# Performance work log

Measured on AMD Instinct MI355X. Metric: run time of the kernel, lower is better.

The kernel has to match this reference:

```python
import jax, jax.numpy as jnp
import numpy as np

B, S, D, H, L = 32, 512, 512, 8, 6
NQ, FF, V, C = 8, 2048, 32000, 10
DK = D // H
EPS = 1e-5


def _layernorm(x, g, b):
    mu = jnp.mean(x, axis=-1, keepdims=True)
    var = jnp.mean(jnp.square(x - mu), axis=-1, keepdims=True)
    return (x - mu) * jax.lax.rsqrt(var + EPS) * g + b


def _pos_encoding(seq_len, dim):
    pos = jnp.arange(seq_len, dtype=jnp.float32)[:, None]
    div = jnp.exp(jnp.arange(0, dim, 2, dtype=jnp.float32) * (-jnp.log(10000.0) / dim))
    pe = jnp.zeros((seq_len, dim), dtype=jnp.float32)
    pe = pe.at[:, 0::2].set(jnp.sin(pos * div))
    pe = pe.at[:, 1::2].set(jnp.cos(pos * div))
    return pe


def setup_inputs() -> dict:
    key = jax.random.key(0)
    ks = jax.random.split(key, 16)
    sd = 0.02
    return {
        "x": jax.random.randint(ks[0], (B, S), 0, V),
        "emb": jax.random.normal(ks[1], (V, D), jnp.float32) * sd,
        "ln1_g": jnp.ones((L, D), jnp.float32),
        "ln1_b": jnp.zeros((L, D), jnp.float32),
        "ln2_g": jnp.ones((L, D), jnp.float32),
        "ln2_b": jnp.zeros((L, D), jnp.float32),
        "attn_w": jax.random.normal(ks[2], (L, D, D), jnp.float32) * sd,
        "attn_b": jnp.zeros((L, D), jnp.float32),
        "theta": jax.random.normal(ks[3], (L, NQ), jnp.float32),
        "ffn_w1": jax.random.normal(ks[4], (L, NQ, FF), jnp.float32) * sd,
        "ffn_b1": jnp.zeros((L, FF), jnp.float32),
        "ffn_w2": jax.random.normal(ks[5], (L, FF, D), jnp.float32) * sd,
        "ffn_b2": jnp.zeros((L, D), jnp.float32),
        "clf_w": jax.random.normal(ks[6], (D, C), jnp.float32) * sd,
        "clf_b": jnp.zeros((C,), jnp.float32),
    }


def reference(x, emb, ln1_g, ln1_b, ln2_g, ln2_b, attn_w, attn_b, theta,
              ffn_w1, ffn_b1, ffn_w2, ffn_b2, clf_w, clf_b):
    h = emb[x] + _pos_encoding(S, D)[None]  # [B,S,D]
    scale = 1.0 / jnp.sqrt(jnp.float32(DK))
    for l in range(L):
        # --- MultiHeadAttentionQuantum: q=k=v=reshape(x), no projections ---
        q = h.reshape(B, S, H, DK)
        scores = jnp.einsum('bihd,bjhd->bhij', q, q) * scale
        p = jax.nn.softmax(scores, axis=-1)
        attn = jnp.einsum('bhij,bjhd->bihd', p, q).reshape(B, S, D)
        attn = attn @ attn_w[l] + attn_b[l]
        h = _layernorm(h + attn, ln1_g[l], ln1_b[l])
        # --- FeedForwardQuantum: per-wire RX-encode -> RY(theta) -> <Z> = cos(x)cos(theta) ---
        qout = jnp.cos(h[..., :NQ]) * jnp.cos(theta[l])  # [B,S,NQ]
        f = jax.nn.relu(qout @ ffn_w1[l] + ffn_b1[l]) @ ffn_w2[l] + ffn_b2[l]
        h = _layernorm(h + f, ln2_g[l], ln2_b[l])
    pooled = jnp.mean(h, axis=1)  # [B,D]
    return pooled @ clf_w + clf_b  # [B,C]
```

## Files before the change

kernel.cpp:

```cpp
#include <hip/hip_runtime.h>
#include <hip/hip_bf16.h>
#include <math.h>

#define BB 32
#define SS 512
#define DD 512
#define HH 8
#define DK 64
#define LL 6
#define NQ 8
#define FF 2048
#define CC 10

typedef unsigned int uint;
typedef unsigned short ushort_t;
using bf16x8 = __attribute__((ext_vector_type(8))) short;
using f32x4  = __attribute__((ext_vector_type(4))) float;

#define MFMA(a, b, c) __builtin_amdgcn_mfma_f32_16x16x32_bf16((a), (b), (c), 0, 0, 0)

union U8 { ushort_t u[8]; bf16x8 v; };

__device__ inline ushort_t f2bf(float x) {
    uint u = __float_as_uint(x);
    u += 0x7FFFu + ((u >> 16) & 1u);
    return (ushort_t)(u >> 16);
}
__device__ inline void tsplit(float v, ushort_t& hi, ushort_t& lo) {
    uint u = __float_as_uint(v);
    hi = (ushort_t)(u >> 16);
    lo = f2bf(v - __uint_as_float(u & 0xFFFF0000u));
}
__device__ inline void tsplit_fast(float v, ushort_t& hi, ushort_t& lo) {
    uint u = __float_as_uint(v);
    hi = (ushort_t)(u >> 16);
    float res = v - __uint_as_float(u & 0xFFFF0000u);
    lo = (ushort_t)(__float_as_uint(res) >> 16);
}
__device__ inline uint packsplit(float v) {
    uint u = __float_as_uint(v) & 0xFFFF0000u;
    uint ru = __float_as_uint(v - __uint_as_float(u));
    ru += 0x7FFFu + ((ru >> 16) & 1u);
    return u | (ru >> 16);
}
__device__ inline float unpackf(uint u) {
    return __uint_as_float(u & 0xFFFF0000u) + __uint_as_float(u << 16);
}

__global__ __launch_bounds__(256) void embed_pe(const int* __restrict__ x,
                                                const float* __restrict__ emb,
                                                uint* __restrict__ Hp) {
    int idx = blockIdx.x * 256 + threadIdx.x;
    if (idx >= BB * SS * DD) return;
    int d = idx & (DD - 1);
    int s = (idx >> 9) & (SS - 1);
    int tok = x[idx >> 9];
    int i2 = d >> 1;
    float freq = expf((float)(2 * i2) * (-9.210340371976184f / (float)DD));
    float ang = (float)s * freq;
    float pe = (d & 1) ? cosf(ang) : sinf(ang);
    Hp[idx] = packsplit(emb[(size_t)tok * DD + d] + pe);
}

__global__ __launch_bounds__(256) void transpose_split_w(const float* __restrict__ in,
                                                         ushort_t* __restrict__ outh,
                                                         ushort_t* __restrict__ outl,
                                                         int K, int N) {
    __shared__ ushort_t th[64][68], tl[64][68];
    int nb = N >> 6;
    int k0 = ((int)blockIdx.x / nb) << 6;
    int n0 = ((int)blockIdx.x % nb) << 6;
    int t = threadIdx.x;
    int r = t >> 2, cb = (t & 3) << 4;
#pragma unroll
    for (int c = 0; c < 4; c++) {
        float4 v = *reinterpret_cast<const float4*>(&in[(size_t)(k0 + r) * N + n0 + cb + 4 * c]);
        float vv[4] = {v.x, v.y, v.z, v.w};
#pragma unroll
        for (int e = 0; e < 4; e++) {
            ushort_t hb, lb; tsplit(vv[e], hb, lb);
            th[r][cb + 4 * c + e] = hb;
            tl[r][cb + 4 * c + e] = lb;
        }
    }
    __syncthreads();
    int n = t >> 2, kb = (t & 3) << 4;
#pragma unroll
    for (int c = 0; c < 4; c++) {
        ushort4 oh, ol;
        oh.x = th[kb + 4 * c + 0][n]; ol.x = tl[kb + 4 * c + 0][n];
        oh.y = th[kb + 4 * c + 1][n]; ol.y = tl[kb + 4 * c + 1][n];
        oh.z = th[kb + 4 * c + 2][n]; ol.z = tl[kb + 4 * c + 2][n];
        oh.w = th[kb + 4 * c + 3][n]; ol.w = tl[kb + 4 * c + 3][n];
        *reinterpret_cast<ushort4*>(&outh[(size_t)(n0 + n) * K + k0 + kb + 4 * c]) = oh;
        *reinterpret_cast<ushort4*>(&outl[(size_t)(n0 + n) * K + k0 + kb + 4 * c]) = ol;
    }
}

__global__ __launch_bounds__(256) void prep_w1t(const float* __restrict__ W1all,
                                                ushort_t* __restrict__ outh,
                                                ushort_t* __restrict__ outl) {
    int l = blockIdx.y;
    int f = blockIdx.x * 256 + threadIdx.x;
    const float* W1 = W1all + (size_t)l * NQ * FF;
    U8 ph, pl;
#pragma unroll
    for (int n = 0; n < 8; n++) {
        ushort_t hb, lb; tsplit(W1[n * FF + f], hb, lb);
        ph.u[n] = hb; pl.u[n] = lb;
    }
    *reinterpret_cast<bf16x8*>(&outh[((size_t)l * FF + f) * 8]) = ph.v;
    *reinterpret_cast<bf16x8*>(&outl[((size_t)l * FF + f) * 8]) = pl.v;
}

__global__ __launch_bounds__(512, 4) void flash_attn_split(const uint* __restrict__ Hp,
                                                           ushort_t* __restrict__ outh,
                                                           ushort_t* __restrict__ outl) {
    __shared__ __align__(16) ushort_t Kh[64][72], Kl[64][72];
    __shared__ __align__(16) ushort_t Vh[64][72], Vl[64][72];
    __shared__ __align__(16) ushort_t Ph[128][72], Pl[128][72];

    int i0 = blockIdx.x * 128;
    int h0 = blockIdx.y * DK;
    int b  = blockIdx.z;
    const uint* baseH = Hp + (size_t)b * (SS * DD);

    int t = threadIdx.x;
    int w = t >> 6;
    int ln = t & 63;
    int l15 = ln & 15, lh = ln >> 4;

    bf16x8 aqh0, aqh1, aql0, aql1;
    {
        int row = i0 + w * 16 + l15;
        const uint* src = &baseH[(size_t)row * DD + h0 + lh * 8];
        uint4 p0 = *reinterpret_cast<const uint4*>(src);
        uint4 p1 = *reinterpret_cast<const uint4*>(src + 4);
        uint4 p2 = *reinterpret_cast<const uint4*>(src + 32);
        uint4 p3 = *reinterpret_cast<const uint4*>(src + 36);
        uint a0[8] = {p0.x, p0.y, p0.z, p0.w, p1.x, p1.y, p1.z, p1.w};
        uint a1[8] = {p2.x, p2.y, p2.z, p2.w, p3.x, p3.y, p3.z, p3.w};
        U8 h0u, l0u, h1u, l1u;
#pragma unroll
        for (int e = 0; e < 8; e++) {
            h0u.u[e] = (ushort_t)(a0[e] >> 16);
            l0u.u[e] = (ushort_t)(a0[e] & 0xFFFFu);
            h1u.u[e] = (ushort_t)(a1[e] >> 16);
            l1u.u[e] = (ushort_t)(a1[e] & 0xFFFFu);
        }
        aqh0 = h0u.v; aql0 = l0u.v; aqh1 = h1u.v; aql1 = l1u.v;
    }

    float m_[4], l_[4], al[4];
    f32x4 acc[4];
    f32x4 z4 = {0.f, 0.f, 0.f, 0.f};
#pragma unroll
    for (int r = 0; r < 4; r++) { m_[r] = -1e30f; l_[r] = 0.f; acc[r] = z4; }

    int kr = t >> 3, kcb = (t & 7) * 8;
    int vc = t & 7, vr = t >> 3;

    for (int j0 = 0; j0 < SS; j0 += 64) {
        __syncthreads();
        {
            const uint* src = &baseH[(size_t)(j0 + kr) * DD + h0 + kcb];
            uint4 p0 = *reinterpret_cast<const uint4*>(src);
            uint4 p1 = *reinterpret_cast<const uint4*>(src + 4);
            uint a[8] = {p0.x, p0.y, p0.z, p0.w, p1.x, p1.y, p1.z, p1.w};
            U8 kh, kl;
#pragma unroll
            for (int e = 0; e < 8; e++) {
                kh.u[e] = (ushort_t)(a[e] >> 16);
                kl.u[e] = (ushort_t)(a[e] & 0xFFFFu);
            }
            *reinterpret_cast<bf16x8*>(&Kh[kr][kcb]) = kh.v;
            *reinterpret_cast<bf16x8*>(&Kl[kr][kcb]) = kl.v;
        }
        __syncthreads();
#pragma unroll
        for (int e = 0; e < 8; e++) {
            int d = vc + 8 * e;
            Vh[d][vr] = Kh[vr][d];
            Vl[d][vr] = Kl[vr][d];
        }
        f32x4 sc[4];
#pragma unroll
        for (int tt = 0; tt < 4; tt++) {
            bf16x8 bh0 = *reinterpret_cast<const bf16x8*>(&Kh[tt * 16 + l15][lh * 8]);
            bf16x8 bh1 = *reinterpret_cast<const bf16x8*>(&Kh[tt * 16 + l15][32 + lh * 8]);
            bf16x8 bl0 = *reinterpret_cast<const bf16x8*>(&Kl[tt * 16 + l15][lh * 8]);
            bf16x8 bl1 = *reinterpret_cast<const bf16x8*>(&Kl[tt * 16 + l15][32 + lh * 8]);
            f32x4 s = z4;
            s = MFMA(aqh0, bh0, s);
            s = MFMA(aqh1, bh1, s);
            s = MFMA(aqh0, bl0, s);
            s = MFMA(aqh1, bl1, s);
            s = MFMA(aql0, bh0, s);
            s = MFMA(aql1, bh1, s);
            sc[tt] = s * 0.125f;
        }
#pragma unroll
        for (int r = 0; r < 4; r++) {
            float mx = fmaxf(fmaxf(sc[0][r], sc[1][r]), fmaxf(sc[2][r], sc[3][r]));
            mx = fmaxf(mx, __shfl_xor(mx, 1));
            mx = fmaxf(mx, __shfl_xor(mx, 2));
            mx = fmaxf(mx, __shfl_xor(mx, 4));
            mx = fmaxf(mx, __shfl_xor(mx, 8));
            float nm = fmaxf(m_[r], mx);
            al[r] = __expf(m_[r] - nm);
            m_[r] = nm;
            float rs = 0.f;
#pragma unroll
            for (int tt = 0; tt < 4; tt++) {
                float p = __expf(sc[tt][r] - nm);
                sc[tt][r] = p;
                rs += p;
            }
            rs += __shfl_xor(rs, 1);
            rs += __shfl_xor(rs, 2);
            rs += __shfl_xor(rs, 4);
            rs += __shfl_xor(rs, 8);
            l_[r] = l_[r] * al[r] + rs;
        }
#pragma unroll
        for (int tt = 0; tt < 4; tt++)
#pragma unroll
            for (int r = 0; r < 4; r++) {
                ushort_t hb, lb; tsplit(sc[tt][r], hb, lb);
                Ph[w * 16 + lh * 4 + r][tt * 16 + l15] = hb;
                Pl[w * 16 + lh * 4 + r][tt * 16 + l15] = lb;
            }
        __syncthreads();
#pragma unroll
        for (int td = 0; td < 4; td++) {
            acc[td][0] *= al[0];
            acc[td][1] *= al[1];
            acc[td][2] *= al[2];
            acc[td][3] *= al[3];
        }
        bf16x8 aph0 = *reinterpret_cast<const bf16x8*>(&Ph[w * 16 + l15][lh * 8]);
        bf16x8 aph1 = *reinterpret_cast<const bf16x8*>(&Ph[w * 16 + l15][32 + lh * 8]);
        bf16x8 apl0 = *reinterpret_cast<const bf16x8*>(&Pl[w * 16 + l15][lh * 8]);
        bf16x8 apl1 = *reinterpret_cast<const bf16x8*>(&Pl[w * 16 + l15][32 + lh * 8]);
#pragma unroll
        for (int td = 0; td < 4; td++) {
            bf16x8 bvh0 = *reinterpret_cast<const bf16x8*>(&Vh[td * 16 + l15][lh * 8]);
            bf16x8 bvh1 = *reinterpret_cast<const bf16x8*>(&Vh[td * 16 + l15][32 + lh * 8]);
            bf16x8 bvl0 = *reinterpret_cast<const bf16x8*>(&Vl[td * 16 + l15][lh * 8]);
            bf16x8 bvl1 = *reinterpret_cast<const bf16x8*>(&Vl[td * 16 + l15][32 + lh * 8]);
            acc[td] = MFMA(aph0, bvh0, acc[td]);
            acc[td] = MFMA(aph1, bvh1, acc[td]);
            acc[td] = MFMA(aph0, bvl0, acc[td]);
            acc[td] = MFMA(aph1, bvl1, acc[td]);
            acc[td] = MFMA(apl0, bvh0, acc[td]);
            acc[td] = MFMA(apl1, bvh1, acc[td]);
        }
    }

#pragma unroll
    for (int r = 0; r < 4; r++) {
        float inv = 1.f / l_[r];
        int row = i0 + w * 16 + lh * 4 + r;
#pragma unroll
        for (int td = 0; td < 4; td++) {
            float o = acc[td][r] * inv;
            ushort_t hb, lb; tsplit(o, hb, lb);
            size_t idx = (size_t)b * SS * DD + (size_t)row * DD + h0 + td * 16 + l15;
            outh[idx] = hb;
            outl[idx] = lb;
        }
    }
}

__global__ __launch_bounds__(512, 4) void gemm_split(const ushort_t* __restrict__ Ah,
                                                     const ushort_t* __restrict__ Al,
                                                     const ushort_t* __restrict__ Bth,
                                                     const ushort_t* __restrict__ Btl,
                                                     const float* __restrict__ bias,
                                                     float* __restrict__ C,
                                                     int M, int N, int K) {
    __shared__ __align__(16) ushort_t Abh[128][72], Abl[128][72];
    __shared__ __align__(16) ushort_t Bbh[128][72], Bbl[128][72];
    int nb = N >> 7;
    int m0 = ((int)blockIdx.x / nb) << 7;
    int n0 = ((int)blockIdx.x % nb) << 7;
    int t = threadIdx.x;
    int w = t >> 6, ln = t & 63, l15 = ln & 15, lh = ln >> 4;
    int wr = (w >> 2) * 64, wc = (w & 3) * 32;

    f32x4 z4 = {0.f, 0.f, 0.f, 0.f};
    f32x4 acc[4][2];
#pragma unroll
    for (int i = 0; i < 4; i++)
#pragma unroll
        for (int j = 0; j < 2; j++) acc[i][j] = z4;

    int arr = t >> 3, akk = (t & 7) * 8;

    for (int k0 = 0; k0 < K; k0 += 64) {
        __syncthreads();
#pragma unroll
        for (int r = 0; r < 2; r++) {
            int row = arr + r * 64;
            *reinterpret_cast<uint4*>(&Abh[row][akk]) =
                *reinterpret_cast<const uint4*>(&Ah[(size_t)(m0 + row) * K + k0 + akk]);
            *reinterpret_cast<uint4*>(&Abl[row][akk]) =
                *reinterpret_cast<const uint4*>(&Al[(size_t)(m0 + row) * K + k0 + akk]);
            *reinterpret_cast<uint4*>(&Bbh[row][akk]) =
                *reinterpret_cast<const uint4*>(&Bth[(size_t)(n0 + row) * K + k0 + akk]);
            *reinterpret_cast<uint4*>(&Bbl[row][akk]) =
                *reinterpret_cast<const uint4*>(&Btl[(size_t)(n0 + row) * K + k0 + akk]);
        }
        __syncthreads();
#pragma unroll
        for (int ks = 0; ks < 2; ks++) {
            bf16x8 ah[4], al_[4];
#pragma unroll
            for (int mt = 0; mt < 4; mt++) {
                ah[mt]  = *reinterpret_cast<const bf16x8*>(&Abh[wr + mt * 16 + l15][ks * 32 + lh * 8]);
                al_[mt] = *reinterpret_cast<const bf16x8*>(&Abl[wr + mt * 16 + l15][ks * 32 + lh * 8]);
            }
#pragma unroll
            for (int nt = 0; nt < 2; nt++) {
                bf16x8 bh = *reinterpret_cast<const bf16x8*>(&Bbh[wc + nt * 16 + l15][ks * 32 + lh * 8]);
                bf16x8 bl = *reinterpret_cast<const bf16x8*>(&Bbl[wc + nt * 16 + l15][ks * 32 + lh * 8]);
#pragma unroll
                for (int mt = 0; mt < 4; mt++) {
                    acc[mt][nt] = MFMA(ah[mt], bh, acc[mt][nt]);
                    acc[mt][nt] = MFMA(ah[mt], bl, acc[mt][nt]);
                    acc[mt][nt] = MFMA(al_[mt], bh, acc[mt][nt]);
                }
            }
        }
    }
#pragma unroll
    for (int nt = 0; nt < 2; nt++) {
        int col = n0 + wc + nt * 16 + l15;
        float bs = bias[col];
#pragma unroll
        for (int mt = 0; mt < 4; mt++)
#pragma unroll
            for (int r = 0; r < 4; r++)
                C[(size_t)(m0 + wr + mt * 16 + lh * 4 + r) * N + col] = acc[mt][nt][r] + bs;
    }
}

__global__ __launch_bounds__(256) void ln_residual(uint* __restrict__ Hp,
                                                   const float* __restrict__ add,
                                                   const float* __restrict__ g,
                                                   const float* __restrict__ bta) {
    int row = blockIdx.x * 4 + (threadIdx.x >> 6);
    int lane = threadIdx.x & 63;
    uint* hp = Hp + (size_t)row * DD;
    const float* ap = add + (size_t)row * DD;
    float v[8];
    float sum = 0.f;
#pragma unroll
    for (int i = 0; i < 8; i++) {
        int d = lane + i * 64;
        v[i] = unpackf(hp[d]) + ap[d];
        sum += v[i];
    }
#pragma unroll
    for (int off = 32; off > 0; off >>= 1) sum += __shfl_xor(sum, off);
    float mu = sum * (1.f / DD);
    float s2 = 0.f;
#pragma unroll
    for (int i = 0; i < 8; i++) {
        float d2 = v[i] - mu;
        s2 += d2 * d2;
    }
#pragma unroll
    for (int off = 32; off > 0; off >>= 1) s2 += __shfl_xor(s2, off);
    float inv = rsqrtf(s2 * (1.f / DD) + 1e-5f);
#pragma unroll
    for (int i = 0; i < 8; i++) {
        int d = lane + i * 64;
        hp[d] = packsplit((v[i] - mu) * inv * g[d] + bta[d]);
    }
}

__global__ __launch_bounds__(512, 4) void ffn_split(const uint* __restrict__ Hp,
                                                    const ushort_t* __restrict__ W1th,
                                                    const ushort_t* __restrict__ W1tl,
                                                    const float* __restrict__ b1,
                                                    const ushort_t* __restrict__ W2th,
                                                    const ushort_t* __restrict__ W2tl,
                                                    const float* __restrict__ b2,
                                                    const float* __restrict__ theta,
                                                    float* __restrict__ outp) {
    __shared__ __align__(16) ushort_t Abh[128][72], Abl[128][72];
    __shared__ __align__(16) ushort_t Bbh[128][72], Bbl[128][72];
    __shared__ __align__(16) ushort_t qsh[129][8], qsl[129][8];
    __shared__ float tcs[8];

    int t = threadIdx.x;
    int m0 = (int)(blockIdx.x >> 2) * 128;
    int n0 = (int)(blockIdx.x & 3) * 128;
    if (t < 8) {
        tcs[t] = cosf(theta[t]);
        qsh[128][t] = 0;
        qsl[128][t] = 0;
    }
    __syncthreads();
#pragma unroll
    for (int i = 0; i < 2; i++) {
        int idx = t + i * 512;
        int m = idx >> 3, n = idx & 7;
        float q = cosf(unpackf(Hp[(size_t)(m0 + m) * DD + n])) * tcs[n];
        ushort_t hb, lb; tsplit(q, hb, lb);
        qsh[m][n] = hb;
        qsl[m][n] = lb;
    }

    int w = t >> 6, ln = t & 63, l15 = ln & 15, lh = ln >> 4;
    int wr = (w >> 2) * 64, wc = (w & 3) * 32;
    bool lh0 = (lh == 0);
    f32x4 z4 = {0.f, 0.f, 0.f, 0.f};
    bf16x8 z8 = {0, 0, 0, 0, 0, 0, 0, 0};
    f32x4 acc[4][2];
#pragma unroll
    for (int i = 0; i < 4; i++)
#pragma unroll
        for (int j = 0; j < 2; j++) acc[i][j] = z4;

    int brr = t >> 3, bkk = (t & 7) * 8;

    for (int k0 = 0; k0 < FF; k0 += 64) {
        __syncthreads();
#pragma unroll
        for (int r = 0; r < 2; r++) {
            int row = brr + r * 64;
            *reinterpret_cast<uint4*>(&Bbh[row][bkk]) =
                *reinterpret_cast<const uint4*>(&W2th[(size_t)(n0 + row) * FF + k0 + bkk]);
            *reinterpret_cast<uint4*>(&Bbl[row][bkk]) =
                *reinterpret_cast<const uint4*>(&W2tl[(size_t)(n0 + row) * FF + k0 + bkk]);
        }
        bf16x8 wh[4], wl[4];
#pragma unroll
        for (int fq = 0; fq < 4; fq++) {
            bf16x8 h8 = *reinterpret_cast<const bf16x8*>(&W1th[(size_t)(k0 + fq * 16 + l15) * 8]);
            bf16x8 l8 = *reinterpret_cast<const bf16x8*>(&W1tl[(size_t)(k0 + fq * 16 + l15) * 8]);
            wh[fq] = lh0 ? h8 : z8;
            wl[fq] = lh0 ? l8 : z8;
        }
        {
            int m = w * 16 + l15;
            int mrow = lh0 ? m : 128;
            bf16x8 qh  = *reinterpret_cast<const bf16x8*>(&qsh[mrow][0]);
            bf16x8 ql_ = *reinterpret_cast<const bf16x8*>(&qsl[mrow][0]);
#pragma unroll
            for (int fq = 0; fq < 4; fq++) {
                f32x4 d = z4;
                d = MFMA(wh[fq], qh, d);
                d = MFMA(wh[fq], ql_, d);
                d = MFMA(wl[fq], qh, d);
                float4 b1v = *reinterpret_cast<const float4*>(&b1[k0 + fq * 16 + lh * 4]);
                float v0 = fmaxf(d[0] + b1v.x, 0.f);
                float v1 = fmaxf(d[1] + b1v.y, 0.f);
                float v2 = fmaxf(d[2] + b1v.z, 0.f);
                float v3 = fmaxf(d[3] + b1v.w, 0.f);
                ushort_t h0_, l0_, h1_, l1_, h2_, l2_, h3_, l3_;
                tsplit_fast(v0, h0_, l0_);
                tsplit_fast(v1, h1_, l1_);
                tsplit_fast(v2, h2_, l2_);
                tsplit_fast(v3, h3_, l3_);
                uint2 hu, lu;
                hu.x = (uint)h0_ | ((uint)h1_ << 16);
                hu.y = (uint)h2_ | ((uint)h3_ << 16);
                lu.x = (uint)l0_ | ((uint)l1_ << 16);
                lu.y = (uint)l2_ | ((uint)l3_ << 16);
                *reinterpret_cast<uint2*>(&Abh[m][fq * 16 + lh * 4]) = hu;
                *reinterpret_cast<uint2*>(&Abl[m][fq * 16 + lh * 4]) = lu;
            }
        }
        __syncthreads();
#pragma unroll
        for (int ks = 0; ks < 2; ks++) {
            bf16x8 ah[4], al_[4];
#pragma unroll
            for (int mt = 0; mt < 4; mt++) {
                ah[mt]  = *reinterpret_cast<const bf16x8*>(&Abh[wr + mt * 16 + l15][ks * 32 + lh * 8]);
                al_[mt] = *reinterpret_cast<const bf16x8*>(&Abl[wr + mt * 16 + l15][ks * 32 + lh * 8]);
            }
#pragma unroll
            for (int nt = 0; nt < 2; nt++) {
                bf16x8 bh = *reinterpret_cast<const bf16x8*>(&Bbh[wc + nt * 16 + l15][ks * 32 + lh * 8]);
                bf16x8 bl = *reinterpret_cast<const bf16x8*>(&Bbl[wc + nt * 16 + l15][ks * 32 + lh * 8]);
#pragma unroll
                for (int mt = 0; mt < 4; mt++) {
                    acc[mt][nt] = MFMA(ah[mt], bh, acc[mt][nt]);
                    acc[mt][nt] = MFMA(ah[mt], bl, acc[mt][nt]);
                    acc[mt][nt] = MFMA(al_[mt], bh, acc[mt][nt]);
                }
            }
        }
    }
#pragma unroll
    for (int nt = 0; nt < 2; nt++) {
        int col = n0 + wc + nt * 16 + l15;
        float bs = b2[col];
#pragma unroll
        for (int mt = 0; mt < 4; mt++)
#pragma unroll
            for (int r = 0; r < 4; r++)
                outp[(size_t)(m0 + wr + mt * 16 + lh * 4 + r) * DD + col] = acc[mt][nt][r] + bs;
    }
}

__global__ __launch_bounds__(256) void pool_mean(const uint* __restrict__ Hp,
                                                 float* __restrict__ pooled) {
    int idx = blockIdx.x * 256 + threadIdx.x;
    if (idx >= BB * DD) return;
    int b = idx >> 9, d = idx & 511;
    float s = 0.f;
    for (int j = 0; j < SS; j++) s += unpackf(Hp[((size_t)b * SS + j) * DD + d]);
    pooled[idx] = s * (1.f / SS);
}

__global__ __launch_bounds__(64) void classifier(const float* __restrict__ pooled,
                                                 const float* __restrict__ W,
                                                 const float* __restrict__ bias,
                                                 float* __restrict__ out) {
    int o = blockIdx.x;
    int b = o / CC, c = o % CC;
    int lane = threadIdx.x;
    float s = 0.f;
    for (int d = lane; d < DD; d += 64) s += pooled[b * DD + d] * W[d * CC + c];
#pragma unroll
    for (int off = 32; off > 0; off >>= 1) s += __shfl_xor(s, off);
    if (lane == 0) out[o] = s + bias[c];
}

extern "C" void kernel_launch(void* const* d_in, const int* in_sizes, int n_in,
                              void* d_out, int out_size, void* d_ws, size_t ws_size,
                              hipStream_t stream) {
    (void)in_sizes; (void)n_in; (void)out_size; (void)ws_size;
    const int*   x      = (const int*)d_in[0];
    const float* emb    = (const float*)d_in[1];
    const float* ln1_g  = (const float*)d_in[2];
    const float* ln1_b  = (const float*)d_in[3];
    const float* ln2_g  = (const float*)d_in[4];
    const float* ln2_b  = (const float*)d_in[5];
    const float* attn_w = (const float*)d_in[6];
    const float* attn_b = (const float*)d_in[7];
    const float* theta  = (const float*)d_in[8];
    const float* ffn_w1 = (const float*)d_in[9];
    const float* ffn_b1 = (const float*)d_in[10];
    const float* ffn_w2 = (const float*)d_in[11];
    const float* ffn_b2 = (const float*)d_in[12];
    const float* clf_w  = (const float*)d_in[13];
    const float* clf_b  = (const float*)d_in[14];
    float* out = (float*)d_out;

    char* ws = (char*)d_ws;
    uint*     Hp     = (uint*)(ws);
    float*    t2     = (float*)(ws + 33554432);
    ushort_t* t1h    = (ushort_t*)(ws + 67108864);
    ushort_t* t1l    = (ushort_t*)(ws + 83886080);
    float*    pooled = (float*)(ws + 100663296);
    ushort_t* Wath   = (ushort_t*)(ws + 100728832);
    ushort_t* Watl   = (ushort_t*)(ws + 101253120);
    ushort_t* W1th6  = (ushort_t*)(ws + 101777408);
    ushort_t* W1tl6  = (ushort_t*)(ws + 101974016);
    ushort_t* W2th   = (ushort_t*)(ws + 67108864);
    ushort_t* W2tl   = (ushort_t*)(ws + 67108864 + 2097152);

    embed_pe<<<(BB * SS * DD + 255) / 256, 256, 0, stream>>>(x, emb, Hp);
    prep_w1t<<<dim3(FF / 256, LL), 256, 0, stream>>>(ffn_w1, W1th6, W1tl6);

    for (int l = 0; l < LL; l++) {
        flash_attn_split<<<dim3(SS / 128, HH, BB), 512, 0, stream>>>(Hp, t1h, t1l);
        transpose_split_w<<<(DD / 64) * (DD / 64), 256, 0, stream>>>(
            attn_w + (size_t)l * DD * DD, Wath, Watl, DD, DD);
        gemm_split<<<(16384 / 128) * (DD / 128), 512, 0, stream>>>(
            t1h, t1l, Wath, Watl, attn_b + l * DD, t2, BB * SS, DD, DD);
        ln_residual<<<BB * SS / 4, 256, 0, stream>>>(Hp, t2, ln1_g + l * DD, ln1_b + l * DD);
        transpose_split_w<<<(FF / 64) * (DD / 64), 256, 0, stream>>>(
            ffn_w2 + (size_t)l * FF * DD, W2th, W2tl, FF, DD);
        ffn_split<<<(16384 / 128) * (DD / 128), 512, 0, stream>>>(
            Hp, W1th6 + (size_t)l * FF * 8, W1tl6 + (size_t)l * FF * 8, ffn_b1 + l * FF,
            W2th, W2tl, ffn_b2 + l * DD, theta + l * NQ, t2);
        ln_residual<<<BB * SS / 4, 256, 0, stream>>>(Hp, t2, ln2_g + l * DD, ln2_b + l * DD);
    }

    pool_mean<<<(BB * DD + 255) / 256, 256, 0, stream>>>(Hp, pooled);
    classifier<<<BB * CC, 64, 0, stream>>>(pooled, clf_w, clf_b, out);
}
```

Measured before the change: 1.883 ms.

## Double-buffer GEMM and FFN tiles with direct global-to-LDS loads and XOR swizzle

```diff
diff --git a/kernel.cpp b/kernel.cpp
--- a/kernel.cpp
+++ b/kernel.cpp
@@ -20,6 +20,12 @@
 #define MFMA(a, b, c) __builtin_amdgcn_mfma_f32_16x16x32_bf16((a), (b), (c), 0, 0, 0)
 
 union U8 { ushort_t u[8]; bf16x8 v; };
+
+__device__ __forceinline__ void gload16(const void* g, void* l) {
+    __builtin_amdgcn_global_load_lds((__attribute__((address_space(1))) void*)g,
+                                     (__attribute__((address_space(3))) void*)l,
+                                     16, 0, 0);
+}
 
 __device__ inline ushort_t f2bf(float x) {
     uint u = __float_as_uint(x);
@@ -272,15 +278,18 @@
     }
 }
 
-__global__ __launch_bounds__(512, 4) void gemm_split(const ushort_t* __restrict__ Ah,
+#define SWZREAD(plane, row, ks) \
+    (*reinterpret_cast<const bf16x8*>(&(plane)[row][((((ks) * 4 + lh) ^ ((row) & 7)) * 8)]))
+
+__global__ __launch_bounds__(512, 2) void gemm_split(const ushort_t* __restrict__ Ah,
                                                      const ushort_t* __restrict__ Al,
                                                      const ushort_t* __restrict__ Bth,
                                                      const ushort_t* __restrict__ Btl,
                                                      const float* __restrict__ bias,
                                                      float* __restrict__ C,
                                                      int M, int N, int K) {
-    __shared__ __align__(16) ushort_t Abh[128][72], Abl[128][72];
-    __shared__ __align__(16) ushort_t Bbh[128][72], Bbl[128][72];
+    __shared__ __align__(16) ushort_t sAh[2][128][64], sAl[2][128][64];
+    __shared__ __align__(16) ushort_t sBh[2][128][64], sBl[2][128][64];
     int nb = N >> 7;
     int m0 = ((int)blockIdx.x / nb) << 7;
     int n0 = ((int)blockIdx.x % nb) << 7;
@@ -295,35 +304,43 @@
 #pragma unroll
         for (int j = 0; j < 2; j++) acc[i][j] = z4;
 
-    int arr = t >> 3, akk = (t & 7) * 8;
-
-    for (int k0 = 0; k0 < K; k0 += 64) {
-        __syncthreads();
-#pragma unroll
-        for (int r = 0; r < 2; r++) {
-            int row = arr + r * 64;
-            *reinterpret_cast<uint4*>(&Abh[row][akk]) =
-                *reinterpret_cast<const uint4*>(&Ah[(size_t)(m0 + row) * K + k0 + akk]);
-            *reinterpret_cast<uint4*>(&Abl[row][akk]) =
-                *reinterpret_cast<const uint4*>(&Al[(size_t)(m0 + row) * K + k0 + akk]);
-            *reinterpret_cast<uint4*>(&Bbh[row][akk]) =
-                *reinterpret_cast<const uint4*>(&Bth[(size_t)(n0 + row) * K + k0 + akk]);
-            *reinterpret_cast<uint4*>(&Bbl[row][akk]) =
-                *reinterpret_cast<const uint4*>(&Btl[(size_t)(n0 + row) * K + k0 + akk]);
-        }
-        __syncthreads();
+    int srow = ln >> 3;
+    int schunk = (ln & 7) ^ srow;
+
+    auto stage = [&](int buf, int kk) {
+#pragma unroll
+        for (int p = 0; p < 2; p++) {
+            int rbase = (w + p * 8) * 8;
+            int grow = rbase + srow;
+            int gc = kk + schunk * 8;
+            gload16(&Ah[(size_t)(m0 + grow) * K + gc],  &sAh[buf][rbase][0]);
+            gload16(&Al[(size_t)(m0 + grow) * K + gc],  &sAl[buf][rbase][0]);
+            gload16(&Bth[(size_t)(n0 + grow) * K + gc], &sBh[buf][rbase][0]);
+            gload16(&Btl[(size_t)(n0 + grow) * K + gc], &sBl[buf][rbase][0]);
+        }
+    };
+
+    stage(0, 0);
+    __syncthreads();
+    int cur = 0;
+    int ntile = K >> 6;
+
+    for (int kt = 0; kt < ntile; kt++) {
+        if (kt + 1 < ntile) stage(cur ^ 1, (kt + 1) * 64);
 #pragma unroll
         for (int ks = 0; ks < 2; ks++) {
             bf16x8 ah[4], al_[4];
 #pragma unroll
             for (int mt = 0; mt < 4; mt++) {
-                ah[mt]  = *reinterpret_cast<const bf16x8*>(&Abh[wr + mt * 16 + l15][ks * 32 + lh * 8]);
-                al_[mt] = *reinterpret_cast<const bf16x8*>(&Abl[wr + mt * 16 + l15][ks * 32 + lh * 8]);
+                int row = wr + mt * 16 + l15;
+                ah[mt]  = SWZREAD(sAh[cur], row, ks);
+                al_[mt] = SWZREAD(sAl[cur], row, ks);
             }
 #pragma unroll
             for (int nt = 0; nt < 2; nt++) {
-                bf16x8 bh = *reinterpret_cast<const bf16x8*>(&Bbh[wc + nt * 16 + l15][ks * 32 + lh * 8]);
-                bf16x8 bl = *reinterpret_cast<const bf16x8*>(&Bbl[wc + nt * 16 + l15][ks * 32 + lh * 8]);
+                int row = wc + nt * 16 + l15;
+                bf16x8 bh = SWZREAD(sBh[cur], row, ks);
+                bf16x8 bl = SWZREAD(sBl[cur], row, ks);
 #pragma unroll
                 for (int mt = 0; mt < 4; mt++) {
                     acc[mt][nt] = MFMA(ah[mt], bh, acc[mt][nt]);
@@ -332,6 +349,8 @@
                 }
             }
         }
+        __syncthreads();
+        cur ^= 1;
     }
 #pragma unroll
     for (int nt = 0; nt < 2; nt++) {
@@ -380,7 +399,7 @@
     }
 }
 
-__global__ __launch_bounds__(512, 4) void ffn_split(const uint* __restrict__ Hp,
+__global__ __launch_bounds__(512, 2) void ffn_split(const uint* __restrict__ Hp,
                                                     const ushort_t* __restrict__ W1th,
                                                     const ushort_t* __restrict__ W1tl,
                                                     const float* __restrict__ b1,
@@ -390,7 +409,7 @@
                                                     const float* __restrict__ theta,
                                                     float* __restrict__ outp) {
     __shared__ __align__(16) ushort_t Abh[128][72], Abl[128][72];
-    __shared__ __align__(16) ushort_t Bbh[128][72], Bbl[128][72];
+    __shared__ __align__(16) ushort_t sBh[2][128][64], sBl[2][128][64];
     __shared__ __align__(16) ushort_t qsh[129][8], qsl[129][8];
     __shared__ float tcs[8];
 
@@ -424,27 +443,38 @@
 #pragma unroll
         for (int j = 0; j < 2; j++) acc[i][j] = z4;
 
-    int brr = t >> 3, bkk = (t & 7) * 8;
+    int srow = ln >> 3;
+    int schunk = (ln & 7) ^ srow;
+
+    auto stageB = [&](int buf, int kk) {
+#pragma unroll
+        for (int p = 0; p < 2; p++) {
+            int rbase = (w + p * 8) * 8;
+            int grow = rbase + srow;
+            int gc = kk + schunk * 8;
+            gload16(&W2th[(size_t)(n0 + grow) * FF + gc], &sBh[buf][rbase][0]);
+            gload16(&W2tl[(size_t)(n0 + grow) * FF + gc], &sBl[buf][rbase][0]);
+        }
+    };
+
+    bf16x8 rwh[4], rwl[4];
+    stageB(0, 0);
+#pragma unroll
+    for (int fq = 0; fq < 4; fq++) {
+        rwh[fq] = *reinterpret_cast<const bf16x8*>(&W1th[(size_t)(fq * 16 + l15) * 8]);
+        rwl[fq] = *reinterpret_cast<const bf16x8*>(&W1tl[(size_t)(fq * 16 + l15) * 8]);
+    }
+    __syncthreads();
+    int cur = 0;
 
     for (int k0 = 0; k0 < FF; k0 += 64) {
-        __syncthreads();
-#pragma unroll
-        for (int r = 0; r < 2; r++) {
-            int row = brr + r * 64;
-            *reinterpret_cast<uint4*>(&Bbh[row][bkk]) =
-                *reinterpret_cast<const uint4*>(&W2th[(size_t)(n0 + row) * FF + k0 + bkk]);
-            *reinterpret_cast<uint4*>(&Bbl[row][bkk]) =
-                *reinterpret_cast<const uint4*>(&W2tl[(size_t)(n0 + row) * FF + k0 + bkk]);
-        }
-        bf16x8 wh[4], wl[4];
-#pragma unroll
-        for (int fq = 0; fq < 4; fq++) {
-            bf16x8 h8 = *reinterpret_cast<const bf16x8*>(&W1th[(size_t)(k0 + fq * 16 + l15) * 8]);
-            bf16x8 l8 = *reinterpret_cast<const bf16x8*>(&W1tl[(size_t)(k0 + fq * 16 + l15) * 8]);
-            wh[fq] = lh0 ? h8 : z8;
-            wl[fq] = lh0 ? l8 : z8;
-        }
         {
+            bf16x8 wh[4], wl[4];
+#pragma unroll
+            for (int fq = 0; fq < 4; fq++) {
+                wh[fq] = lh0 ? rwh[fq] : z8;
+                wl[fq] = lh0 ? rwl[fq] : z8;
+            }
             int m = w * 16 + l15;
             int mrow = lh0 ? m : 128;
             bf16x8 qh  = *reinterpret_cast<const bf16x8*>(&qsh[mrow][0]);
@@ -475,6 +505,15 @@
             }
         }
         __syncthreads();
+        if (k0 + 64 < FF) {
+            int k1 = k0 + 64;
+            stageB(cur ^ 1, k1);
+#pragma unroll
+            for (int fq = 0; fq < 4; fq++) {
+                rwh[fq] = *reinterpret_cast<const bf16x8*>(&W1th[(size_t)(k1 + fq * 16 + l15) * 8]);
+                rwl[fq] = *reinterpret_cast<const bf16x8*>(&W1tl[(size_t)(k1 + fq * 16 + l15) * 8]);
+            }
+        }
 #pragma unroll
         for (int ks = 0; ks < 2; ks++) {
             bf16x8 ah[4], al_[4];
@@ -485,8 +524,9 @@
             }
 #pragma unroll
             for (int nt = 0; nt < 2; nt++) {
-                bf16x8 bh = *reinterpret_cast<const bf16x8*>(&Bbh[wc + nt * 16 + l15][ks * 32 + lh * 8]);
-                bf16x8 bl = *reinterpret_cast<const bf16x8*>(&Bbl[wc + nt * 16 + l15][ks * 32 + lh * 8]);
+                int row = wc + nt * 16 + l15;
+                bf16x8 bh = SWZREAD(sBh[cur], row, ks);
+                bf16x8 bl = SWZREAD(sBl[cur], row, ks);
 #pragma unroll
                 for (int mt = 0; mt < 4; mt++) {
                     acc[mt][nt] = MFMA(ah[mt], bh, acc[mt][nt]);
@@ -495,6 +535,8 @@
                 }
             }
         }
+        __syncthreads();
+        cur ^= 1;
     }
 #pragma unroll
     for (int nt = 0; nt < 2; nt++) {
```

Result: slower. 1.994 ms (+5.9%).
